# Kernel optimization log

Hardware: AMD Instinct MI355X
Metric: run time of the kernel (lower is better)

## Reference

```python
import jax, jax.numpy as jnp
import numpy as np

D = 128
B = 512
N = 512
MAX_HOPS = 3


def _masked_softmax(v, mask, axis):
    m = jnp.max(v, axis=axis, keepdims=True)
    e = jnp.exp(v - m) * mask
    s = jnp.sum(e, axis=axis, keepdims=True) + 1e-5
    return e / s


def _l2_norm(x):
    # torch renorm(p=2, dim=0, maxnorm=1e-12).mul(1e12): rows with norm>maxnorm -> x/norm,
    # rows with norm<=maxnorm stay unchanged then *1e12
    maxnorm = 1e-12
    norm = jnp.sqrt(jnp.sum(x * x, axis=1, keepdims=True))
    safe = jnp.maximum(norm, maxnorm)
    return jnp.where(norm > maxnorm, x / safe, x * (1.0 / maxnorm))


def setup_inputs() -> dict:
    key = jax.random.key(0)
    ks = jax.random.split(key, 12)
    xavier = lambda k, shp: jax.random.uniform(k, shp, jnp.float32, -1.0, 1.0) * np.sqrt(6.0 / (shp[0] + shp[1]))
    return {
        "e1_embeded": jax.random.normal(ks[0], (B, D), jnp.float32),
        "rel_embeded": jax.random.normal(ks[1], (B, D), jnp.float32),
        "nei_embeded_key": jax.random.normal(ks[2], (B, N, D), jnp.float32),
        "nei_embeded_value": jax.random.normal(ks[3], (B, N, D), jnp.float32),
        "nei_mask": jax.random.randint(ks[4], (B, N), 0, 2, jnp.int32),
        "Wk": xavier(ks[5], (D, D)),
        "Wv": xavier(ks[6], (D, D)),
        "W_lin": xavier(ks[7], (D, D)),
        "b_lin": jnp.zeros((D,), jnp.float32),
        "W_att": xavier(ks[8], (3 * D, D)),
        "b_att": jnp.zeros((D,), jnp.float32),
        "dim": 2,
    }


def reference(e1_embeded, rel_embeded, nei_embeded_key, nei_embeded_value, nei_mask,
              Wk, Wv, W_lin, b_lin, W_att, b_att, dim):
    mask = nei_mask.astype(jnp.float32)  # [B,N]
    fk = jnp.einsum('bnd,de->bne', nei_embeded_key * mask[..., None], Wk)   # [B,N,D]
    fv = jnp.einsum('bnd,de->bne', nei_embeded_value * mask[..., None], Wv)  # [B,N,D]
    n = fk.shape[1]
    rel_b = jnp.broadcast_to(rel_embeded[:, None, :], fk.shape)
    u = e1_embeded
    for _ in range(MAX_HOPS):
        u_batch = jax.nn.leaky_relu(u @ W_lin + b_lin)                      # [B,D]
        ent_b = jnp.broadcast_to(u[:, None, :], fk.shape)
        m = jnp.concatenate([fk, ent_b, rel_b], axis=2)                      # [B,N,3D]
        att = jnp.sum(jax.nn.leaky_relu(jnp.einsum('bnk,kd->bnd', m, W_att) + b_att), axis=2)  # [B,N]
        p = _masked_softmax(att, mask, axis=1)
        o = jnp.sum(fv * p[..., None], axis=1)                               # [B,D]
        u = _l2_norm(u_batch + o)
    return u
```

## Files before the change

### kernel.cpp

```cpp
#include <hip/hip_runtime.h>

#define D 128
#define NN 512
#define BB 512

typedef __attribute__((ext_vector_type(8))) short short8;
typedef __attribute__((ext_vector_type(4))) float f32x4;

__device__ __forceinline__ unsigned int fbits(float f) {
  union { float f; unsigned int u; } v; v.f = f; return v.u;
}
__device__ __forceinline__ float ubits(unsigned int u) {
  union { unsigned int u; float f; } v; v.u = u; return v.f;
}
__device__ __forceinline__ unsigned short f2bf(float f) {
  unsigned int x = fbits(f);
  return (unsigned short)((x + 0x7fffu + ((x >> 16) & 1u)) >> 16);
}
__device__ __forceinline__ float h2f(unsigned short u) {
  _Float16 h; __builtin_memcpy(&h, &u, 2); return (float)h;
}
__device__ __forceinline__ unsigned short f2h(float f) {
  _Float16 h = (_Float16)f; unsigned short u; __builtin_memcpy(&u, &h, 2); return u;
}
__device__ __forceinline__ float lrelu(float x) { return x > 0.f ? x : 0.01f * x; }

__device__ __forceinline__ int fragidx(int k, int n) {
  return ((((n >> 4) * 4 + (k >> 5)) * 64 + ((k >> 3) & 3) * 16 + (n & 15)) << 3) + (k & 7);
}

__global__ __launch_bounds__(256) void prep_kernel(
    const float* __restrict__ Wk, const float* __restrict__ Watt,
    const float* __restrict__ batt, const float* __restrict__ rel,
    unsigned short* __restrict__ WhF, unsigned short* __restrict__ WlF,
    float* __restrict__ c3) {
  __shared__ float rowS[D];
  __shared__ float psum[2][D];
  const int blk = blockIdx.x;
  const int t = threadIdx.x;
  const float* src = (blk < D) ? (Wk + blk * D) : (rel + (blk - D) * D);
  const float* W   = (blk < D) ? Watt : (Watt + 2 * D * D);
  if (t < D) rowS[t] = src[t];
  __syncthreads();
  const int d = t & 127, half = t >> 7;
  const float* Wp = W + (half * 64) * D + d;
  float a = 0.f;
  #pragma unroll 8
  for (int k = 0; k < 64; ++k) a += rowS[half * 64 + k] * Wp[k * D];
  psum[half][d] = a;
  __syncthreads();
  if (t < D) {
    const float w = psum[0][t] + psum[1][t];
    if (blk < D) {
      const unsigned int ub = fbits(w);
      const int idx = fragidx(blk, t);
      WhF[idx] = (unsigned short)(ub >> 16);
      WlF[idx] = f2bf(w - ubits(ub & 0xFFFF0000u));
    } else {
      c3[(blk - D) * D + t] = w + batt[t];
    }
  }
}

__global__ __launch_bounds__(256) void gemm_g1_kernel(
    const float* __restrict__ key, const int* __restrict__ mask,
    const unsigned short* __restrict__ WhF, const unsigned short* __restrict__ WlF,
    unsigned short* __restrict__ g1h) {
  __shared__ __align__(16) unsigned short whlds[8192];
  __shared__ __align__(16) unsigned short wllds[8192];
  const int t = threadIdx.x;
  const int ch = blockIdx.x & 1;
  const unsigned short* Wh = WhF + ch * 8192;
  const unsigned short* Wl = WlF + ch * 8192;
  #pragma unroll
  for (int i = 0; i < 4; ++i) {
    const int unit = t + i * 256;
    *reinterpret_cast<uint4*>(&whlds[unit * 8]) = *reinterpret_cast<const uint4*>(Wh + unit * 8);
    *reinterpret_cast<uint4*>(&wllds[unit * 8]) = *reinterpret_cast<const uint4*>(Wl + unit * 8);
  }
  __syncthreads();
  const int wave = t >> 6, lane = t & 63;
  const int q = lane >> 4, l15 = lane & 15;
  const int nrt = (BB * NN) / 64;
  const int rstride = gridDim.x >> 1;
  for (int rt = blockIdx.x >> 1; rt < nrt; rt += rstride) {
    const long rowbase = (long)rt * 64 + wave * 16;
    const long r = rowbase + l15;
    const int mk = mask[r];
    f32x4 acc[4];
    #pragma unroll
    for (int c = 0; c < 4; ++c) acc[c] = (f32x4){0.f, 0.f, 0.f, 0.f};
    #pragma unroll
    for (int kt = 0; kt < 4; ++kt) {
      const float* kp = key + r * D + kt * 32 + q * 8;
      float xs[8];
      *reinterpret_cast<float4*>(&xs[0]) = *reinterpret_cast<const float4*>(kp);
      *reinterpret_cast<float4*>(&xs[4]) = *reinterpret_cast<const float4*>(kp + 4);
      union { unsigned int u[4]; short8 v; } cvh, cvl;
      #pragma unroll
      for (int p2 = 0; p2 < 4; ++p2) {
        float a = xs[2 * p2], b = xs[2 * p2 + 1];
        if (!mk) { a = 0.f; b = 0.f; }
        const unsigned int ua = fbits(a), ub = fbits(b);
        cvh.u[p2] = (ua >> 16) | (ub & 0xFFFF0000u);
        const float ra = a - ubits(ua & 0xFFFF0000u);
        const float rb = b - ubits(ub & 0xFFFF0000u);
        cvl.u[p2] = (unsigned int)f2bf(ra) | ((unsigned int)f2bf(rb) << 16);
      }
      const short8 ah = cvh.v, al = cvl.v;
      #pragma unroll
      for (int c = 0; c < 4; ++c) {
        const short8 bh = *reinterpret_cast<const short8*>(&whlds[((c * 4 + kt) * 64 + lane) * 8]);
        const short8 bl = *reinterpret_cast<const short8*>(&wllds[((c * 4 + kt) * 64 + lane) * 8]);
        acc[c] = __builtin_amdgcn_mfma_f32_16x16x32_bf16(ah, bh, acc[c], 0, 0, 0);
        acc[c] = __builtin_amdgcn_mfma_f32_16x16x32_bf16(al, bh, acc[c], 0, 0, 0);
        acc[c] = __builtin_amdgcn_mfma_f32_16x16x32_bf16(ah, bl, acc[c], 0, 0, 0);
      }
    }
    const int4 mr4 = *reinterpret_cast<const int4*>(mask + rowbase + q * 4);
    const int mrr[4] = {mr4.x, mr4.y, mr4.z, mr4.w};
    #pragma unroll
    for (int c = 0; c < 4; ++c) {
      #pragma unroll
      for (int reg = 0; reg < 4; ++reg) {
        if (mrr[reg]) {
          const long row = rowbase + q * 4 + reg;
          g1h[row * D + ch * 64 + c * 16 + l15] = f2h(acc[c][reg]);
        }
      }
    }
  }
}

__global__ __launch_bounds__(512, 2) void hops_kernel(
    const float* __restrict__ e1, const int* __restrict__ mask,
    const float* __restrict__ value, const unsigned short* __restrict__ g1h,
    const float* __restrict__ Wlin, const float* __restrict__ blin,
    const float* __restrict__ Watt, const float* __restrict__ Wv,
    const float* __restrict__ c3, float* __restrict__ out) {
  __shared__ float uS[D], cS[D], ubS[D], opS[D];
  __shared__ float attS[NN];
  __shared__ float part[4][D];
  __shared__ float oscr[8][D];
  __shared__ float redA[8], redB[8];
  __shared__ int idxS[NN];
  __shared__ int redI[8];
  __shared__ int padRowS;
  const int b = blockIdx.x;
  const int t = threadIdx.x;
  const int wv = t >> 6, lane = t & 63;
  const int grp = t >> 4, l = t & 15, d0 = (t & 15) * 8;
  const long base = (long)b * NN * D;
  const int* mb = mask + b * NN;
  if (t < D) uS[t] = e1[b * D + t];
  const int myMask = mb[t];
  {
    const unsigned long long bal = __ballot(myMask != 0);
    const int lanePre = __popcll(bal & ((1ULL << lane) - 1ULL));
    if (lane == 0) redI[wv] = __popcll(bal);
    if (!myMask) padRowS = t;
    __syncthreads();
    int wbase = 0, cnt = 0;
    #pragma unroll
    for (int w2 = 0; w2 < 8; ++w2) {
      const int c = redI[w2];
      if (w2 < wv) wbase += c;
      cnt += c;
    }
    if (myMask) idxS[wbase + lanePre] = t;
    const int cntPad = (cnt + 127) & ~127;
    __syncthreads();
    for (int i = cnt + t; i < cntPad; i += 512) idxS[i] = padRowS;
    redI[0] = cntPad >> 7;
    __syncthreads();
  }
  const int nb = redI[0];
  float4 va0[4], vb0[4], va1[4], vb1[4];
  if (nb > 0) {
    #pragma unroll
    for (int j2 = 0; j2 < 4; ++j2) {
      const int n = idxS[j2 * 32 + grp];
      const float* vp = value + base + (long)n * D + d0;
      va0[j2] = *reinterpret_cast<const float4*>(vp);
      vb0[j2] = *reinterpret_cast<const float4*>(vp + 4);
    }
  }
  if (nb > 1) {
    #pragma unroll
    for (int j2 = 0; j2 < 4; ++j2) {
      const int n = idxS[128 + j2 * 32 + grp];
      const float* vp = value + base + (long)n * D + d0;
      va1[j2] = *reinterpret_cast<const float4*>(vp);
      vb1[j2] = *reinterpret_cast<const float4*>(vp + 4);
    }
  }
  for (int hop = 0; hop < 3; ++hop) {
    {
      const int d = t & 127, role = t >> 7;
      const float* W = (role < 2) ? (Watt + D * D) : Wlin;
      const int k0 = (role & 1) * 64;
      const float* Wp = W + k0 * D + d;
      float a = 0.f;
      #pragma unroll 8
      for (int k = 0; k < 64; ++k) a += uS[k0 + k] * Wp[k * D];
      part[role][d] = a;
    }
    __syncthreads();
    if (t < D) cS[t] = part[0][t] + part[1][t] + c3[b * D + t];
    else if (t < 2 * D) { const int d = t - D; ubS[d] = lrelu(part[2][d] + part[3][d] + blin[d]); }
    __syncthreads();
    if (t < 128) {
      float v = lrelu(cS[t]);
      #pragma unroll
      for (int off = 32; off > 0; off >>= 1) v += __shfl_xor(v, off, 64);
      if (lane == 0) redB[wv] = v;
    }
    {
      float creg[8];
      #pragma unroll
      for (int j = 0; j < 8; ++j) creg[j] = cS[d0 + j];
      for (int ii = 0; ii < nb; ++ii) {
        int ns[4]; uint4 g[4];
        #pragma unroll
        for (int j2 = 0; j2 < 4; ++j2) ns[j2] = idxS[ii * 128 + j2 * 32 + grp];
        #pragma unroll
        for (int j2 = 0; j2 < 4; ++j2)
          g[j2] = *reinterpret_cast<const uint4*>(g1h + base + (long)ns[j2] * D + d0);
        #pragma unroll
        for (int j2 = 0; j2 < 4; ++j2) {
          const unsigned short* e = reinterpret_cast<const unsigned short*>(&g[j2]);
          float s = 0.f;
          #pragma unroll
          for (int j = 0; j < 8; ++j) s += lrelu(h2f(e[j]) + creg[j]);
          #pragma unroll
          for (int off = 8; off > 0; off >>= 1) s += __shfl_xor(s, off, 16);
          if (l == 0) attS[ns[j2]] = s;
        }
      }
    }
    __syncthreads();
    {
      const float av = myMask ? attS[t] : (redB[0] + redB[1]);
      float m = av;
      #pragma unroll
      for (int off = 32; off > 0; off >>= 1) m = fmaxf(m, __shfl_xor(m, off, 64));
      if (lane == 0) redA[wv] = m;
      __syncthreads();
      m = redA[0];
      #pragma unroll
      for (int w2 = 1; w2 < 8; ++w2) m = fmaxf(m, redA[w2]);
      const float e0 = __expf(av - m) * (myMask ? 1.f : 0.f);
      float ss = e0;
      #pragma unroll
      for (int off = 32; off > 0; off >>= 1) ss += __shfl_xor(ss, off, 64);
      if (lane == 0) redB[wv] = ss;
      __syncthreads();
      float s = 1e-5f;
      #pragma unroll
      for (int w2 = 0; w2 < 8; ++w2) s += redB[w2];
      attS[t] = e0 / s;
    }
    __syncthreads();
    {
      float acc8[8];
      #pragma unroll
      for (int j = 0; j < 8; ++j) acc8[j] = 0.f;
      if (nb > 0) {
        #pragma unroll
        for (int j2 = 0; j2 < 4; ++j2) {
          const float p = attS[idxS[j2 * 32 + grp]];
          acc8[0] += p * va0[j2].x; acc8[1] += p * va0[j2].y;
          acc8[2] += p * va0[j2].z; acc8[3] += p * va0[j2].w;
          acc8[4] += p * vb0[j2].x; acc8[5] += p * vb0[j2].y;
          acc8[6] += p * vb0[j2].z; acc8[7] += p * vb0[j2].w;
        }
      }
      if (nb > 1) {
        #pragma unroll
        for (int j2 = 0; j2 < 4; ++j2) {
          const float p = attS[idxS[128 + j2 * 32 + grp]];
          acc8[0] += p * va1[j2].x; acc8[1] += p * va1[j2].y;
          acc8[2] += p * va1[j2].z; acc8[3] += p * va1[j2].w;
          acc8[4] += p * vb1[j2].x; acc8[5] += p * vb1[j2].y;
          acc8[6] += p * vb1[j2].z; acc8[7] += p * vb1[j2].w;
        }
      }
      for (int ii = 2; ii < nb; ++ii) {
        int ns[4]; float4 va[4], vb[4];
        #pragma unroll
        for (int j2 = 0; j2 < 4; ++j2) ns[j2] = idxS[ii * 128 + j2 * 32 + grp];
        #pragma unroll
        for (int j2 = 0; j2 < 4; ++j2) {
          const float* vp = value + base + (long)ns[j2] * D + d0;
          va[j2] = *reinterpret_cast<const float4*>(vp);
          vb[j2] = *reinterpret_cast<const float4*>(vp + 4);
        }
        #pragma unroll
        for (int j2 = 0; j2 < 4; ++j2) {
          const float p = attS[ns[j2]];
          acc8[0] += p * va[j2].x; acc8[1] += p * va[j2].y;
          acc8[2] += p * va[j2].z; acc8[3] += p * va[j2].w;
          acc8[4] += p * vb[j2].x; acc8[5] += p * vb[j2].y;
          acc8[6] += p * vb[j2].z; acc8[7] += p * vb[j2].w;
        }
      }
      #pragma unroll
      for (int j = 0; j < 8; ++j) {
        acc8[j] += __shfl_xor(acc8[j], 16, 64);
        acc8[j] += __shfl_xor(acc8[j], 32, 64);
      }
      if (lane < 16) {
        #pragma unroll
        for (int j = 0; j < 8; ++j) oscr[wv][lane * 8 + j] = acc8[j];
      }
    }
    __syncthreads();
    if (t < D) {
      float s = 0.f;
      #pragma unroll
      for (int w2 = 0; w2 < 8; ++w2) s += oscr[w2][t];
      opS[t] = s;
    }
    __syncthreads();
    {
      const int d = t & 127, role = t >> 7;
      const int k0 = role * 32;
      const float* Wp = Wv + k0 * D + d;
      float a = 0.f;
      #pragma unroll 8
      for (int k = 0; k < 32; ++k) a += opS[k0 + k] * Wp[k * D];
      part[role][d] = a;
    }
    __syncthreads();
    {
      float un = 0.f, sq = 0.f;
      if (t < D) {
        un = ubS[t] + part[0][t] + part[1][t] + part[2][t] + part[3][t];
        sq = un * un;
      }
      #pragma unroll
      for (int off = 32; off > 0; off >>= 1) sq += __shfl_xor(sq, off, 64);
      if (lane == 0) redA[wv] = sq;
      __syncthreads();
      float ns = 0.f;
      #pragma unroll
      for (int w2 = 0; w2 < 8; ++w2) ns += redA[w2];
      const float norm = sqrtf(ns);
      const float inv = (norm > 1e-12f) ? (1.f / norm) : 1e12f;
      if (t < D) uS[t] = un * inv;
    }
    __syncthreads();
  }
  if (t < D) out[b * D + t] = uS[t];
}

extern "C" void kernel_launch(void* const* d_in, const int* in_sizes, int n_in,
                              void* d_out, int out_size, void* d_ws, size_t ws_size,
                              hipStream_t stream) {
  const float* e1   = (const float*)d_in[0];
  const float* rel  = (const float*)d_in[1];
  const float* key  = (const float*)d_in[2];
  const float* val  = (const float*)d_in[3];
  const int*   mask = (const int*)d_in[4];
  const float* Wk   = (const float*)d_in[5];
  const float* Wv   = (const float*)d_in[6];
  const float* Wlin = (const float*)d_in[7];
  const float* blin = (const float*)d_in[8];
  const float* Watt = (const float*)d_in[9];
  const float* batt = (const float*)d_in[10];
  float* out = (float*)d_out;

  char* ws = (char*)d_ws;
  unsigned short* WhF = (unsigned short*)ws;
  unsigned short* WlF = (unsigned short*)(ws + 32 * 1024);
  float*          c3  = (float*)(ws + 64 * 1024);
  unsigned short* g1h = (unsigned short*)(ws + 512 * 1024);

  prep_kernel<<<D + BB, 256, 0, stream>>>(Wk, Watt, batt, rel, WhF, WlF, c3);
  gemm_g1_kernel<<<2048, 256, 0, stream>>>(key, mask, WhF, WlF, g1h);
  hops_kernel<<<BB, 512, 0, stream>>>(e1, mask, val, g1h, Wlin, blin, Watt, Wv, c3, out);
}
```

Baseline: 362.0 us.

## Cache value rows as packed fp16 in registers and raise occupancy target

The hops kernel used to preload the first two chunks of value rows as fp32 float4 registers before the hop loop. Now hop 0 loads them on the fly and stores fp16-packed copies, which halves the register footprint. Hops 1 and 2 reuse these packed copies. Launch bounds go from 2 to 4 blocks per CU, trading register budget for occupancy, with some added fp16 rounding error in the value accumulation and a risk of spills.

New measurement: 352.9 us. 1.03x faster.

```diff
diff --git a/kernel.cpp b/kernel.cpp
--- a/kernel.cpp
+++ b/kernel.cpp
@@ -132,7 +132,7 @@
   }
 }
 
-__global__ __launch_bounds__(512, 2) void hops_kernel(
+__global__ __launch_bounds__(512, 4) void hops_kernel(
     const float* __restrict__ e1, const int* __restrict__ mask,
     const float* __restrict__ value, const unsigned short* __restrict__ g1h,
     const float* __restrict__ Wlin, const float* __restrict__ blin,
@@ -175,26 +175,9 @@
     __syncthreads();
   }
   const int nb = redI[0];
-  float4 va0[4], vb0[4], va1[4], vb1[4];
-  if (nb > 0) {
-    #pragma unroll
-    for (int j2 = 0; j2 < 4; ++j2) {
-      const int n = idxS[j2 * 32 + grp];
-      const float* vp = value + base + (long)n * D + d0;
-      va0[j2] = *reinterpret_cast<const float4*>(vp);
-      vb0[j2] = *reinterpret_cast<const float4*>(vp + 4);
-    }
-  }
-  if (nb > 1) {
-    #pragma unroll
-    for (int j2 = 0; j2 < 4; ++j2) {
-      const int n = idxS[128 + j2 * 32 + grp];
-      const float* vp = value + base + (long)n * D + d0;
-      va1[j2] = *reinterpret_cast<const float4*>(vp);
-      vb1[j2] = *reinterpret_cast<const float4*>(vp + 4);
-    }
-  }
-  for (int hop = 0; hop < 3; ++hop) {
+  uint4 kv0[4], kv1[4];
+
+  auto phases123 = [&]() {
     {
       const int d = t & 127, role = t >> 7;
       const float* W = (role < 2) ? (Watt + D * D) : Wlin;
@@ -207,7 +190,7 @@
     }
     __syncthreads();
     if (t < D) cS[t] = part[0][t] + part[1][t] + c3[b * D + t];
-    else if (t < 2 * D) { const int d = t - D; ubS[d] = lrelu(part[2][d] + part[3][d] + blin[d]); }
+    else if (t < 2 * D) { const int d2 = t - D; ubS[d2] = lrelu(part[2][d2] + part[3][d2] + blin[d2]); }
     __syncthreads();
     if (t < 128) {
       float v = lrelu(cS[t]);
@@ -261,58 +244,37 @@
       attS[t] = e0 / s;
     }
     __syncthreads();
-    {
-      float acc8[8];
-      #pragma unroll
-      for (int j = 0; j < 8; ++j) acc8[j] = 0.f;
-      if (nb > 0) {
-        #pragma unroll
-        for (int j2 = 0; j2 < 4; ++j2) {
-          const float p = attS[idxS[j2 * 32 + grp]];
-          acc8[0] += p * va0[j2].x; acc8[1] += p * va0[j2].y;
-          acc8[2] += p * va0[j2].z; acc8[3] += p * va0[j2].w;
-          acc8[4] += p * vb0[j2].x; acc8[5] += p * vb0[j2].y;
-          acc8[6] += p * vb0[j2].z; acc8[7] += p * vb0[j2].w;
-        }
-      }
-      if (nb > 1) {
-        #pragma unroll
-        for (int j2 = 0; j2 < 4; ++j2) {
-          const float p = attS[idxS[128 + j2 * 32 + grp]];
-          acc8[0] += p * va1[j2].x; acc8[1] += p * va1[j2].y;
-          acc8[2] += p * va1[j2].z; acc8[3] += p * va1[j2].w;
-          acc8[4] += p * vb1[j2].x; acc8[5] += p * vb1[j2].y;
-          acc8[6] += p * vb1[j2].z; acc8[7] += p * vb1[j2].w;
-        }
-      }
-      for (int ii = 2; ii < nb; ++ii) {
-        int ns[4]; float4 va[4], vb[4];
-        #pragma unroll
-        for (int j2 = 0; j2 < 4; ++j2) ns[j2] = idxS[ii * 128 + j2 * 32 + grp];
-        #pragma unroll
-        for (int j2 = 0; j2 < 4; ++j2) {
-          const float* vp = value + base + (long)ns[j2] * D + d0;
-          va[j2] = *reinterpret_cast<const float4*>(vp);
-          vb[j2] = *reinterpret_cast<const float4*>(vp + 4);
-        }
-        #pragma unroll
-        for (int j2 = 0; j2 < 4; ++j2) {
-          const float p = attS[ns[j2]];
-          acc8[0] += p * va[j2].x; acc8[1] += p * va[j2].y;
-          acc8[2] += p * va[j2].z; acc8[3] += p * va[j2].w;
-          acc8[4] += p * vb[j2].x; acc8[5] += p * vb[j2].y;
-          acc8[6] += p * vb[j2].z; acc8[7] += p * vb[j2].w;
-        }
-      }
-      #pragma unroll
-      for (int j = 0; j < 8; ++j) {
-        acc8[j] += __shfl_xor(acc8[j], 16, 64);
-        acc8[j] += __shfl_xor(acc8[j], 32, 64);
-      }
-      if (lane < 16) {
-        #pragma unroll
-        for (int j = 0; j < 8; ++j) oscr[wv][lane * 8 + j] = acc8[j];
-      }
+  };
+  auto loadTail4 = [&](float (&acc8)[8]) {
+    for (int ii = 2; ii < nb; ++ii) {
+      int ns[4]; float4 va[4], vb[4];
+      #pragma unroll
+      for (int j2 = 0; j2 < 4; ++j2) ns[j2] = idxS[ii * 128 + j2 * 32 + grp];
+      #pragma unroll
+      for (int j2 = 0; j2 < 4; ++j2) {
+        const float* vp = value + base + (long)ns[j2] * D + d0;
+        va[j2] = *reinterpret_cast<const float4*>(vp);
+        vb[j2] = *reinterpret_cast<const float4*>(vp + 4);
+      }
+      #pragma unroll
+      for (int j2 = 0; j2 < 4; ++j2) {
+        const float p = attS[ns[j2]];
+        acc8[0] += p * va[j2].x; acc8[1] += p * va[j2].y;
+        acc8[2] += p * va[j2].z; acc8[3] += p * va[j2].w;
+        acc8[4] += p * vb[j2].x; acc8[5] += p * vb[j2].y;
+        acc8[6] += p * vb[j2].z; acc8[7] += p * vb[j2].w;
+      }
+    }
+  };
+  auto finishTail = [&](float (&acc8)[8]) {
+    #pragma unroll
+    for (int j = 0; j < 8; ++j) {
+      acc8[j] += __shfl_xor(acc8[j], 16, 64);
+      acc8[j] += __shfl_xor(acc8[j], 32, 64);
+    }
+    if (lane < 16) {
+      #pragma unroll
+      for (int j = 0; j < 8; ++j) oscr[wv][lane * 8 + j] = acc8[j];
     }
     __syncthreads();
     if (t < D) {
@@ -342,14 +304,101 @@
       for (int off = 32; off > 0; off >>= 1) sq += __shfl_xor(sq, off, 64);
       if (lane == 0) redA[wv] = sq;
       __syncthreads();
-      float ns = 0.f;
-      #pragma unroll
-      for (int w2 = 0; w2 < 8; ++w2) ns += redA[w2];
-      const float norm = sqrtf(ns);
+      float ns2 = 0.f;
+      #pragma unroll
+      for (int w2 = 0; w2 < 8; ++w2) ns2 += redA[w2];
+      const float norm = sqrtf(ns2);
       const float inv = (norm > 1e-12f) ? (1.f / norm) : 1e12f;
       if (t < D) uS[t] = un * inv;
     }
     __syncthreads();
+  };
+
+  phases123();
+  {
+    float acc8[8];
+    #pragma unroll
+    for (int j = 0; j < 8; ++j) acc8[j] = 0.f;
+    if (nb > 0) {
+      float4 va[4], vb[4];
+      #pragma unroll
+      for (int j2 = 0; j2 < 4; ++j2) {
+        const float* vp = value + base + (long)idxS[j2 * 32 + grp] * D + d0;
+        va[j2] = *reinterpret_cast<const float4*>(vp);
+        vb[j2] = *reinterpret_cast<const float4*>(vp + 4);
+      }
+      #pragma unroll
+      for (int j2 = 0; j2 < 4; ++j2) {
+        const float p = attS[idxS[j2 * 32 + grp]];
+        acc8[0] += p * va[j2].x; acc8[1] += p * va[j2].y;
+        acc8[2] += p * va[j2].z; acc8[3] += p * va[j2].w;
+        acc8[4] += p * vb[j2].x; acc8[5] += p * vb[j2].y;
+        acc8[6] += p * vb[j2].z; acc8[7] += p * vb[j2].w;
+        kv0[j2].x = (unsigned)f2h(va[j2].x) | ((unsigned)f2h(va[j2].y) << 16);
+        kv0[j2].y = (unsigned)f2h(va[j2].z) | ((unsigned)f2h(va[j2].w) << 16);
+        kv0[j2].z = (unsigned)f2h(vb[j2].x) | ((unsigned)f2h(vb[j2].y) << 16);
+        kv0[j2].w = (unsigned)f2h(vb[j2].z) | ((unsigned)f2h(vb[j2].w) << 16);
+      }
+    }
+    if (nb > 1) {
+      float4 va[4], vb[4];
+      #pragma unroll
+      for (int j2 = 0; j2 < 4; ++j2) {
+        const float* vp = value + base + (long)idxS[128 + j2 * 32 + grp] * D + d0;
+        va[j2] = *reinterpret_cast<const float4*>(vp);
+        vb[j2] = *reinterpret_cast<const float4*>(vp + 4);
+      }
+      #pragma unroll
+      for (int j2 = 0; j2 < 4; ++j2) {
+        const float p = attS[idxS[128 + j2 * 32 + grp]];
+        acc8[0] += p * va[j2].x; acc8[1] += p * va[j2].y;
+        acc8[2] += p * va[j2].z; acc8[3] += p * va[j2].w;
+        acc8[4] += p * vb[j2].x; acc8[5] += p * vb[j2].y;
+        acc8[6] += p * vb[j2].z; acc8[7] += p * vb[j2].w;
+        kv1[j2].x = (unsigned)f2h(va[j2].x) | ((unsigned)f2h(va[j2].y) << 16);
+        kv1[j2].y = (unsigned)f2h(va[j2].z) | ((unsigned)f2h(va[j2].w) << 16);
+        kv1[j2].z = (unsigned)f2h(vb[j2].x) | ((unsigned)f2h(vb[j2].y) << 16);
+        kv1[j2].w = (unsigned)f2h(vb[j2].z) | ((unsigned)f2h(vb[j2].w) << 16);
+      }
+    }
+    loadTail4(acc8);
+    finishTail(acc8);
+  }
+  for (int hop = 1; hop < 3; ++hop) {
+    phases123();
+    float acc8[8];
+    #pragma unroll
+    for (int j = 0; j < 8; ++j) acc8[j] = 0.f;
+    if (nb > 0) {
+      #pragma unroll
+      for (int j2 = 0; j2 < 4; ++j2) {
+        const float p = attS[idxS[j2 * 32 + grp]];
+        acc8[0] += p * h2f((unsigned short)(kv0[j2].x & 0xffffu));
+        acc8[1] += p * h2f((unsigned short)(kv0[j2].x >> 16));
+        acc8[2] += p * h2f((unsigned short)(kv0[j2].y & 0xffffu));
+        acc8[3] += p * h2f((unsigned short)(kv0[j2].y >> 16));
+        acc8[4] += p * h2f((unsigned short)(kv0[j2].z & 0xffffu));
+        acc8[5] += p * h2f((unsigned short)(kv0[j2].z >> 16));
+        acc8[6] += p * h2f((unsigned short)(kv0[j2].w & 0xffffu));
+        acc8[7] += p * h2f((unsigned short)(kv0[j2].w >> 16));
+      }
+    }
+    if (nb > 1) {
+      #pragma unroll
+      for (int j2 = 0; j2 < 4; ++j2) {
+        const float p = attS[idxS[128 + j2 * 32 + grp]];
+        acc8[0] += p * h2f((unsigned short)(kv1[j2].x & 0xffffu));
+        acc8[1] += p * h2f((unsigned short)(kv1[j2].x >> 16));
+        acc8[2] += p * h2f((unsigned short)(kv1[j2].y & 0xffffu));
+        acc8[3] += p * h2f((unsigned short)(kv1[j2].y >> 16));
+        acc8[4] += p * h2f((unsigned short)(kv1[j2].z & 0xffffu));
+        acc8[5] += p * h2f((unsigned short)(kv1[j2].z >> 16));
+        acc8[6] += p * h2f((unsigned short)(kv1[j2].w & 0xffffu));
+        acc8[7] += p * h2f((unsigned short)(kv1[j2].w >> 16));
+      }
+    }
+    loadTail4(acc8);
+    finishTail(acc8);
   }
   if (t < D) out[b * D + t] = uS[t];
 }
```

## Drop persistent value-register cache, prefetch per hop, and raise occupancy

Applied to the files above, without the earlier changes.

The kernel no longer keeps the first 256 value rows in registers across all hops. Each hop now prefetches the first two g1h chunks before the matvec, and the first value chunk after the attention scores are computed. This lowers register pressure so the launch bounds can request 4 blocks per SM instead of 2, and the small matvec unroll factors are raised to 16. In exchange, value rows are reloaded every hop, which adds global traffic, and the kernel may spill if the tighter register budget cannot be met.

Result: slower. 475.3 us (+31.3%).

```diff
diff --git a/kernel.cpp b/kernel.cpp
--- a/kernel.cpp
+++ b/kernel.cpp
@@ -132,7 +132,7 @@
   }
 }
 
-__global__ __launch_bounds__(512, 2) void hops_kernel(
+__global__ __launch_bounds__(512, 4) void hops_kernel(
     const float* __restrict__ e1, const int* __restrict__ mask,
     const float* __restrict__ value, const unsigned short* __restrict__ g1h,
     const float* __restrict__ Wlin, const float* __restrict__ blin,
@@ -175,33 +175,25 @@
     __syncthreads();
   }
   const int nb = redI[0];
-  float4 va0[4], vb0[4], va1[4], vb1[4];
-  if (nb > 0) {
-    #pragma unroll
-    for (int j2 = 0; j2 < 4; ++j2) {
-      const int n = idxS[j2 * 32 + grp];
-      const float* vp = value + base + (long)n * D + d0;
-      va0[j2] = *reinterpret_cast<const float4*>(vp);
-      vb0[j2] = *reinterpret_cast<const float4*>(vp + 4);
-    }
-  }
-  if (nb > 1) {
-    #pragma unroll
-    for (int j2 = 0; j2 < 4; ++j2) {
-      const int n = idxS[128 + j2 * 32 + grp];
-      const float* vp = value + base + (long)n * D + d0;
-      va1[j2] = *reinterpret_cast<const float4*>(vp);
-      vb1[j2] = *reinterpret_cast<const float4*>(vp + 4);
-    }
-  }
   for (int hop = 0; hop < 3; ++hop) {
+    uint4 pg0[4], pg1[4];
+    if (nb > 0) {
+      #pragma unroll
+      for (int j2 = 0; j2 < 4; ++j2)
+        pg0[j2] = *reinterpret_cast<const uint4*>(g1h + base + (long)idxS[j2 * 32 + grp] * D + d0);
+    }
+    if (nb > 1) {
+      #pragma unroll
+      for (int j2 = 0; j2 < 4; ++j2)
+        pg1[j2] = *reinterpret_cast<const uint4*>(g1h + base + (long)idxS[128 + j2 * 32 + grp] * D + d0);
+    }
     {
       const int d = t & 127, role = t >> 7;
       const float* W = (role < 2) ? (Watt + D * D) : Wlin;
       const int k0 = (role & 1) * 64;
       const float* Wp = W + k0 * D + d;
       float a = 0.f;
-      #pragma unroll 8
+      #pragma unroll 16
       for (int k = 0; k < 64; ++k) a += uS[k0 + k] * Wp[k * D];
       part[role][d] = a;
     }
@@ -219,7 +211,33 @@
       float creg[8];
       #pragma unroll
       for (int j = 0; j < 8; ++j) creg[j] = cS[d0 + j];
-      for (int ii = 0; ii < nb; ++ii) {
+      if (nb > 0) {
+        #pragma unroll
+        for (int j2 = 0; j2 < 4; ++j2) {
+          const int n = idxS[j2 * 32 + grp];
+          const unsigned short* e = reinterpret_cast<const unsigned short*>(&pg0[j2]);
+          float s = 0.f;
+          #pragma unroll
+          for (int j = 0; j < 8; ++j) s += lrelu(h2f(e[j]) + creg[j]);
+          #pragma unroll
+          for (int off = 8; off > 0; off >>= 1) s += __shfl_xor(s, off, 16);
+          if (l == 0) attS[n] = s;
+        }
+      }
+      if (nb > 1) {
+        #pragma unroll
+        for (int j2 = 0; j2 < 4; ++j2) {
+          const int n = idxS[128 + j2 * 32 + grp];
+          const unsigned short* e = reinterpret_cast<const unsigned short*>(&pg1[j2]);
+          float s = 0.f;
+          #pragma unroll
+          for (int j = 0; j < 8; ++j) s += lrelu(h2f(e[j]) + creg[j]);
+          #pragma unroll
+          for (int off = 8; off > 0; off >>= 1) s += __shfl_xor(s, off, 16);
+          if (l == 0) attS[n] = s;
+        }
+      }
+      for (int ii = 2; ii < nb; ++ii) {
         int ns[4]; uint4 g[4];
         #pragma unroll
         for (int j2 = 0; j2 < 4; ++j2) ns[j2] = idxS[ii * 128 + j2 * 32 + grp];
@@ -236,6 +254,15 @@
           for (int off = 8; off > 0; off >>= 1) s += __shfl_xor(s, off, 16);
           if (l == 0) attS[ns[j2]] = s;
         }
+      }
+    }
+    float4 pva[4], pvb[4];
+    if (nb > 0) {
+      #pragma unroll
+      for (int j2 = 0; j2 < 4; ++j2) {
+        const float* vp = value + base + (long)idxS[j2 * 32 + grp] * D + d0;
+        pva[j2] = *reinterpret_cast<const float4*>(vp);
+        pvb[j2] = *reinterpret_cast<const float4*>(vp + 4);
       }
     }
     __syncthreads();
@@ -269,23 +296,13 @@
         #pragma unroll
         for (int j2 = 0; j2 < 4; ++j2) {
           const float p = attS[idxS[j2 * 32 + grp]];
-          acc8[0] += p * va0[j2].x; acc8[1] += p * va0[j2].y;
-          acc8[2] += p * va0[j2].z; acc8[3] += p * va0[j2].w;
-          acc8[4] += p * vb0[j2].x; acc8[5] += p * vb0[j2].y;
-          acc8[6] += p * vb0[j2].z; acc8[7] += p * vb0[j2].w;
-        }
-      }
-      if (nb > 1) {
-        #pragma unroll
-        for (int j2 = 0; j2 < 4; ++j2) {
-          const float p = attS[idxS[128 + j2 * 32 + grp]];
-          acc8[0] += p * va1[j2].x; acc8[1] += p * va1[j2].y;
-          acc8[2] += p * va1[j2].z; acc8[3] += p * va1[j2].w;
-          acc8[4] += p * vb1[j2].x; acc8[5] += p * vb1[j2].y;
-          acc8[6] += p * vb1[j2].z; acc8[7] += p * vb1[j2].w;
-        }
-      }
-      for (int ii = 2; ii < nb; ++ii) {
+          acc8[0] += p * pva[j2].x; acc8[1] += p * pva[j2].y;
+          acc8[2] += p * pva[j2].z; acc8[3] += p * pva[j2].w;
+          acc8[4] += p * pvb[j2].x; acc8[5] += p * pvb[j2].y;
+          acc8[6] += p * pvb[j2].z; acc8[7] += p * pvb[j2].w;
+        }
+      }
+      for (int ii = 1; ii < nb; ++ii) {
         int ns[4]; float4 va[4], vb[4];
         #pragma unroll
         for (int j2 = 0; j2 < 4; ++j2) ns[j2] = idxS[ii * 128 + j2 * 32 + grp];
@@ -327,7 +344,7 @@
       const int k0 = role * 32;
       const float* Wp = Wv + k0 * D + d;
       float a = 0.f;
-      #pragma unroll 8
+      #pragma unroll 16
       for (int k = 0; k < 32; ++k) a += opS[k0 + k] * Wp[k * D];
       part[role][d] = a;
     }
```
